# Kernel tuning notes

Hardware: AMD Instinct MI355X
Metric: run time of the kernel (lower is better)

Reference implementation:

```python
import jax, jax.numpy as jnp
import numpy as np

N_NODES = 100000


def gcn_conv(x, edge_index, W, b, num_nodes):
    """PyG GCNConv: y = D^{-1/2} (A + I) D^{-1/2} (x W) + b.

    edge_index[0] = source (row), edge_index[1] = target (col);
    messages flow source -> target with symmetric normalization.
    """
    # add self loops
    loop = jnp.arange(num_nodes, dtype=edge_index.dtype)
    row = jnp.concatenate([edge_index[0], loop])  # [E+N]
    col = jnp.concatenate([edge_index[1], loop])  # [E+N]

    xw = x @ W  # [N, F_out] -- tiny GEMM, done before gather

    # degree of target nodes (incl. self loops)
    ones = jnp.ones(col.shape[0], dtype=x.dtype)
    deg = jax.ops.segment_sum(ones, col, num_segments=num_nodes)  # [N]
    dis = jax.lax.rsqrt(jnp.maximum(deg, 1e-12))
    dis = jnp.where(deg > 0, dis, 0.0)

    norm = dis[row] * dis[col]  # [E+N]
    msg = xw[row] * norm[:, None]  # gather + scale, [E+N, F_out]
    out = jax.ops.segment_sum(msg, col, num_segments=num_nodes)  # scatter-add
    return out + b


def setup_inputs() -> dict:
    key = jax.random.key(0)
    k1, k2, k3, k4 = jax.random.split(key, 4)
    num_attr, hidden, num_classes = 128, 16, 8
    n_edges = 3200000
    x = jax.random.normal(k1, (N_NODES, num_attr), dtype=jnp.float32)
    edge_index = jax.random.randint(k2, (2, n_edges), 0, N_NODES, dtype=jnp.int64)
    W1 = jax.random.normal(k3, (num_attr, hidden), dtype=jnp.float32) / np.sqrt(num_attr)
    b1 = jnp.zeros((hidden,), dtype=jnp.float32)
    W2 = jax.random.normal(k4, (hidden, num_classes), dtype=jnp.float32) / np.sqrt(hidden)
    b2 = jnp.zeros((num_classes,), dtype=jnp.float32)
    return {"x": x, "edge_index": edge_index, "W1": W1, "b1": b1, "W2": W2, "b2": b2}


def reference(x, edge_index, W1, b1, W2, b2):
    h = gcn_conv(x, edge_index, W1, b1, N_NODES)
    h = jax.nn.relu(h)
    # dropout is identity in eval mode
    h = gcn_conv(h, edge_index, W2, b2, N_NODES)
    return jax.nn.sigmoid(h)  # [N, num_classes]
```

## Files before the change

kernel.cpp:

```cpp
#include <hip/hip_runtime.h>
#include <math.h>

static constexpr int FI = 128;
static constexpr int FH = 16;
static constexpr int FO = 8;

static constexpr int BIN_SHIFT = 8;
static constexpr int BIN_NODES = 256;
static constexpr int MAX_BINS  = 512;
static constexpr int CAPB      = 8832;
static constexpr int SCHUNK    = 8192;
static constexpr int SThreads  = 512;

__device__ __forceinline__ unsigned short f2bf(float x) {
    unsigned u = __float_as_uint(x);
    u += 0x7FFFu + ((u >> 16) & 1u);
    return (unsigned short)(u >> 16);
}
__device__ __forceinline__ float bflo(unsigned u) { return __uint_as_float(u << 16); }
__device__ __forceinline__ float bfhi(unsigned u) { return __uint_as_float(u & 0xFFFF0000u); }

__launch_bounds__(SThreads)
__global__ void k_binscatter(const int* __restrict__ row, const int* __restrict__ col,
                             int* __restrict__ binCursor, unsigned int* __restrict__ binned,
                             int E, int nbins) {
    __shared__ int lcnt[MAX_BINS];
    __shared__ int lstart[MAX_BINS];
    __shared__ int lcur[MAX_BINS];
    __shared__ int gbase[MAX_BINS];
    __shared__ int wsum[8];
    __shared__ unsigned int   staged[SCHUNK];
    __shared__ unsigned short sbin[SCHUNK];
    int t = threadIdx.x;
    int base = blockIdx.x * SCHUNK;
    int end  = base + SCHUNK; if (end > E) end = E;
    int m = end - base;
    lcnt[t] = 0;
    __syncthreads();

    int nv = m >> 2;
    const int4* c4 = (const int4*)(col + base);
    int4 creg[4];
    #pragma unroll
    for (int j = 0; j < 4; ++j) {
        int k = t + j * SThreads;
        if (k < nv) {
            creg[j] = c4[k];
            atomicAdd(&lcnt[creg[j].x >> BIN_SHIFT], 1);
            atomicAdd(&lcnt[creg[j].y >> BIN_SHIFT], 1);
            atomicAdd(&lcnt[creg[j].z >> BIN_SHIFT], 1);
            atomicAdd(&lcnt[creg[j].w >> BIN_SHIFT], 1);
        }
    }
    for (int i = base + (nv << 2) + t; i < end; i += SThreads)
        atomicAdd(&lcnt[col[i] >> BIN_SHIFT], 1);
    __syncthreads();

    int v = lcnt[t];
    int inc = v;
    #pragma unroll
    for (int d = 1; d < 64; d <<= 1) {
        int u = __shfl_up(inc, d, 64);
        if ((t & 63) >= d) inc += u;
    }
    if ((t & 63) == 63) wsum[t >> 6] = inc;
    __syncthreads();
    if (t < 8) {
        int w = wsum[t];
        #pragma unroll
        for (int d = 1; d < 8; d <<= 1) {
            int u = __shfl_up(w, d, 8);
            if (t >= d) w += u;
        }
        wsum[t] = w;
    }
    __syncthreads();
    {
        int waveoff = (t >= 64) ? wsum[(t >> 6) - 1] : 0;
        int ex = waveoff + inc - v;
        lstart[t] = ex;
        lcur[t]   = ex;
        gbase[t]  = v ? atomicAdd(&binCursor[t], v) : 0;
    }
    __syncthreads();

    const int4* r4 = (const int4*)(row + base);
    #pragma unroll
    for (int j = 0; j < 4; ++j) {
        int k = t + j * SThreads;
        if (k < nv) {
            int4 r = r4[k];
            int cc[4] = {creg[j].x, creg[j].y, creg[j].z, creg[j].w};
            int rr[4] = {r.x, r.y, r.z, r.w};
            #pragma unroll
            for (int jj = 0; jj < 4; ++jj) {
                int b = cc[jj] >> BIN_SHIFT;
                int pos = atomicAdd(&lcur[b], 1);
                staged[pos] = (unsigned)rr[jj] | ((unsigned)(cc[jj] & (BIN_NODES - 1)) << 17);
                sbin[pos] = (unsigned short)b;
            }
        }
    }
    for (int i = base + (nv << 2) + t; i < end; i += SThreads) {
        int c = col[i];
        int b = c >> BIN_SHIFT;
        int pos = atomicAdd(&lcur[b], 1);
        staged[pos] = (unsigned)row[i] | ((unsigned)(c & (BIN_NODES - 1)) << 17);
        sbin[pos] = (unsigned short)b;
    }
    __syncthreads();

    for (int i = t; i < m; i += SThreads) {
        int b = sbin[i];
        int off = gbase[b] + (i - lstart[b]);
        if (off < CAPB) binned[b * CAPB + off] = staged[i];
    }
}

__launch_bounds__(BIN_NODES)
__global__ void k_refine(const int* __restrict__ binCursor, const unsigned int* __restrict__ binned,
                         int* __restrict__ srow, int* __restrict__ starts, int* __restrict__ ends,
                         float* __restrict__ dis, int N) {
    __shared__ unsigned int  stage[CAPB];
    __shared__ unsigned char arr[CAPB];
    __shared__ int cnt[BIN_NODES];
    __shared__ int wsum[4];
    int t = threadIdx.x;
    int b = blockIdx.x;
    int s = b * CAPB;
    int m = binCursor[b];
    if (m > CAPB) m = CAPB;
    cnt[t] = 0;
    __syncthreads();

    int mm = m & ~3;
    for (int i0 = t * 4; i0 < mm; i0 += BIN_NODES * 4) {
        uint4 v = *(const uint4*)(binned + s + i0);
        *(uint4*)&stage[i0] = v;
        arr[i0 + 0] = (unsigned char)atomicAdd(&cnt[v.x >> 17], 1);
        arr[i0 + 1] = (unsigned char)atomicAdd(&cnt[v.y >> 17], 1);
        arr[i0 + 2] = (unsigned char)atomicAdd(&cnt[v.z >> 17], 1);
        arr[i0 + 3] = (unsigned char)atomicAdd(&cnt[v.w >> 17], 1);
    }
    for (int i = mm + t; i < m; i += BIN_NODES) {
        unsigned v = binned[s + i];
        stage[i] = v;
        arr[i] = (unsigned char)atomicAdd(&cnt[v >> 17], 1);
    }
    __syncthreads();

    int deg = cnt[t];
    int inc = deg;
    #pragma unroll
    for (int d = 1; d < 64; d <<= 1) {
        int u = __shfl_up(inc, d, 64);
        if ((t & 63) >= d) inc += u;
    }
    if ((t & 63) == 63) wsum[t >> 6] = inc;
    __syncthreads();
    if (t < 4) {
        int w = wsum[t];
        #pragma unroll
        for (int d = 1; d < 4; d <<= 1) {
            int u = __shfl_up(w, d, 4);
            if (t >= d) w += u;
        }
        wsum[t] = w;
    }
    __syncthreads();
    int waveoff = (t >= 64) ? wsum[(t >> 6) - 1] : 0;
    int excl = waveoff + inc - deg;

    int n = b * BIN_NODES + t;
    if (n < N) {
        starts[n] = s + excl;
        ends[n]   = s + excl + deg;
        dis[n]    = rsqrtf((float)(deg + 1));
    }
    cnt[t] = excl;
    __syncthreads();

    for (int i0 = t * 4; i0 < mm; i0 += BIN_NODES * 4) {
        uint4 v = *(uint4*)&stage[i0];
        srow[s + cnt[v.x >> 17] + arr[i0 + 0]] = v.x & 0x1FFFF;
        srow[s + cnt[v.y >> 17] + arr[i0 + 1]] = v.y & 0x1FFFF;
        srow[s + cnt[v.z >> 17] + arr[i0 + 2]] = v.z & 0x1FFFF;
        srow[s + cnt[v.w >> 17] + arr[i0 + 3]] = v.w & 0x1FFFF;
    }
    for (int i = mm + t; i < m; i += BIN_NODES) {
        unsigned v = stage[i];
        srow[s + cnt[v >> 17] + arr[i]] = v & 0x1FFFF;
    }
}

__launch_bounds__(256)
__global__ void k_gemm1(const float* __restrict__ x, const float* __restrict__ W,
                        const float* __restrict__ dis, unsigned short* __restrict__ xw1s,
                        int N) {
    __shared__ float sw[FI * FH];
    int t = threadIdx.x;
    for (int i = t; i < FI * FH; i += 256) sw[i] = W[i];
    __syncthreads();

    int nl = t >> 2;
    int f  = (t & 3) * 4;
    int n  = blockIdx.x * 64 + nl;
    if (n >= N) return;

    const float4* xr = (const float4*)(x + (size_t)n * FI);
    float a0 = 0.f, a1 = 0.f, a2 = 0.f, a3 = 0.f;
    #pragma unroll 8
    for (int kq = 0; kq < FI / 4; ++kq) {
        float4 xv = xr[kq];
        float4 w0 = *(const float4*)&sw[(kq * 4 + 0) * FH + f];
        float4 w1 = *(const float4*)&sw[(kq * 4 + 1) * FH + f];
        float4 w2 = *(const float4*)&sw[(kq * 4 + 2) * FH + f];
        float4 w3 = *(const float4*)&sw[(kq * 4 + 3) * FH + f];
        a0 = fmaf(xv.x, w0.x, a0); a1 = fmaf(xv.x, w0.y, a1);
        a2 = fmaf(xv.x, w0.z, a2); a3 = fmaf(xv.x, w0.w, a3);
        a0 = fmaf(xv.y, w1.x, a0); a1 = fmaf(xv.y, w1.y, a1);
        a2 = fmaf(xv.y, w1.z, a2); a3 = fmaf(xv.y, w1.w, a3);
        a0 = fmaf(xv.z, w2.x, a0); a1 = fmaf(xv.z, w2.y, a1);
        a2 = fmaf(xv.z, w2.z, a2); a3 = fmaf(xv.z, w2.w, a3);
        a0 = fmaf(xv.w, w3.x, a0); a1 = fmaf(xv.w, w3.y, a1);
        a2 = fmaf(xv.w, w3.z, a2); a3 = fmaf(xv.w, w3.w, a3);
    }
    float dn = dis[n];
    unsigned w0 = (unsigned)f2bf(a0 * dn) | ((unsigned)f2bf(a1 * dn) << 16);
    unsigned w1 = (unsigned)f2bf(a2 * dn) | ((unsigned)f2bf(a3 * dn) << 16);
    *(uint2*)(xw1s + (size_t)n * FH + f) = make_uint2(w0, w1);
}

__launch_bounds__(256)
__global__ void k_agg1(const int* __restrict__ starts, const int* __restrict__ ends,
                       const int* __restrict__ srow, const float* __restrict__ dis,
                       const unsigned short* __restrict__ xw1s, const float* __restrict__ W2,
                       const float* __restrict__ b1, unsigned short* __restrict__ xw2s, int N) {
    __shared__ float sw[FH * FO];
    __shared__ float sb[FH];
    int t = threadIdx.x;
    if (t < FH * FO) sw[t] = W2[t];
    if (t < FH) sb[t] = b1[t];
    __syncthreads();

    int n = blockIdx.x * 128 + (t >> 1);
    int h = t & 1;
    if (n >= N) return;
    float dn = dis[n];
    int s = starts[n], e = ends[n];
    const uint4* xq = (const uint4*)xw1s;

    uint4 sp = xq[(size_t)n * 2 + h];
    float acc[8];
    acc[0]=bflo(sp.x); acc[1]=bfhi(sp.x); acc[2]=bflo(sp.y); acc[3]=bfhi(sp.y);
    acc[4]=bflo(sp.z); acc[5]=bfhi(sp.z); acc[6]=bflo(sp.w); acc[7]=bfhi(sp.w);

    int i = s;
    for (; i + 8 <= e; i += 8) {
        int rr[8];
        #pragma unroll
        for (int j = 0; j < 8; ++j) rr[j] = srow[i + j];
        uint4 pk[8];
        #pragma unroll
        for (int j = 0; j < 8; ++j) pk[j] = xq[(size_t)rr[j] * 2 + h];
        #pragma unroll
        for (int j = 0; j < 8; ++j) {
            acc[0]+=bflo(pk[j].x); acc[1]+=bfhi(pk[j].x);
            acc[2]+=bflo(pk[j].y); acc[3]+=bfhi(pk[j].y);
            acc[4]+=bflo(pk[j].z); acc[5]+=bfhi(pk[j].z);
            acc[6]+=bflo(pk[j].w); acc[7]+=bfhi(pk[j].w);
        }
    }
    for (; i < e; ++i) {
        uint4 p = xq[(size_t)srow[i] * 2 + h];
        acc[0]+=bflo(p.x); acc[1]+=bfhi(p.x);
        acc[2]+=bflo(p.y); acc[3]+=bfhi(p.y);
        acc[4]+=bflo(p.z); acc[5]+=bfhi(p.z);
        acc[6]+=bflo(p.w); acc[7]+=bfhi(p.w);
    }

    float hv[8];
    #pragma unroll
    for (int k = 0; k < 8; ++k) {
        float v = fmaf(dn, acc[k], sb[h * 8 + k]);
        hv[k] = v > 0.f ? v : 0.f;
    }
    float po[FO];
    #pragma unroll
    for (int o = 0; o < FO; ++o) {
        float a = 0.f;
        #pragma unroll
        for (int k = 0; k < 8; ++k) a = fmaf(hv[k], sw[(h * 8 + k) * FO + o], a);
        po[o] = a;
    }
    #pragma unroll
    for (int o = 0; o < FO; ++o) po[o] += __shfl_xor(po[o], 1, 64);
    int o0 = h * 4;
    unsigned w0 = (unsigned)f2bf(po[o0 + 0] * dn) | ((unsigned)f2bf(po[o0 + 1] * dn) << 16);
    unsigned w1 = (unsigned)f2bf(po[o0 + 2] * dn) | ((unsigned)f2bf(po[o0 + 3] * dn) << 16);
    *(uint2*)(xw2s + (size_t)n * FO + o0) = make_uint2(w0, w1);
}

__launch_bounds__(256)
__global__ void k_agg2(const int* __restrict__ starts, const int* __restrict__ ends,
                       const int* __restrict__ srow, const float* __restrict__ dis,
                       const unsigned short* __restrict__ xw2s, const float* __restrict__ b2,
                       float* __restrict__ out, int N) {
    int t = threadIdx.x;
    int n = blockIdx.x * 128 + (t >> 1);
    int h = t & 1;
    if (n >= N) return;
    float dn = dis[n];
    int s = starts[n], e = ends[n];
    const uint2* xq = (const uint2*)xw2s;

    uint2 sp = xq[(size_t)n * 2 + h];
    float acc[4];
    acc[0]=bflo(sp.x); acc[1]=bfhi(sp.x); acc[2]=bflo(sp.y); acc[3]=bfhi(sp.y);

    int i = s;
    for (; i + 8 <= e; i += 8) {
        int rr[8];
        #pragma unroll
        for (int j = 0; j < 8; ++j) rr[j] = srow[i + j];
        uint2 pk[8];
        #pragma unroll
        for (int j = 0; j < 8; ++j) pk[j] = xq[(size_t)rr[j] * 2 + h];
        #pragma unroll
        for (int j = 0; j < 8; ++j) {
            acc[0]+=bflo(pk[j].x); acc[1]+=bfhi(pk[j].x);
            acc[2]+=bflo(pk[j].y); acc[3]+=bfhi(pk[j].y);
        }
    }
    for (; i < e; ++i) {
        uint2 p = xq[(size_t)srow[i] * 2 + h];
        acc[0]+=bflo(p.x); acc[1]+=bfhi(p.x);
        acc[2]+=bflo(p.y); acc[3]+=bfhi(p.y);
    }

    int f0 = h * 4;
    float r[4];
    #pragma unroll
    for (int k = 0; k < 4; ++k) {
        float v = fmaf(dn, acc[k], b2[f0 + k]);
        r[k] = 1.f / (1.f + __expf(-v));
    }
    *(float4*)(out + (size_t)n * FO + f0) = make_float4(r[0], r[1], r[2], r[3]);
}

extern "C" void kernel_launch(void* const* d_in, const int* in_sizes, int n_in,
                              void* d_out, int out_size, void* d_ws, size_t ws_size,
                              hipStream_t stream) {
    const float* x  = (const float*)d_in[0];
    const int*   ei = (const int*)d_in[1];
    const float* W1 = (const float*)d_in[2];
    const float* b1 = (const float*)d_in[3];
    const float* W2 = (const float*)d_in[4];
    const float* b2 = (const float*)d_in[5];

    const int N = in_sizes[0] / FI;
    const int E = in_sizes[1] / 2;
    const int* row = ei;
    const int* col = ei + E;
    const int nbins = (N + BIN_NODES - 1) >> BIN_SHIFT;

    const size_t NP = 100352;
    const size_t BINSZ = (size_t)nbins * CAPB;
    float* base = (float*)d_ws;
    int*   starts    = (int*)base;
    int*   ends      = (int*)(base + NP);
    float* dis       = base + 2 * NP;
    int*   binCursor = (int*)(base + 3 * NP);
    unsigned int* binned = (unsigned int*)(base + 3 * NP + 1024);
    int*   srow      = (int*)(base + 3 * NP + 1024 + BINSZ);
    unsigned short* xw1s = (unsigned short*)(base + 3 * NP + 1024 + 2 * BINSZ);
    unsigned short* xw2s = (unsigned short*)(base + 3 * NP + 1024 + 2 * BINSZ + NP * 8);
    float* out = (float*)d_out;

    size_t needed = (3 * NP + 1024 + 2 * BINSZ + NP * 12) * 4;
    if (ws_size < needed) return;

    hipMemsetAsync(binCursor, 0, (size_t)nbins * sizeof(int), stream);
    k_binscatter<<<(E + SCHUNK - 1) / SCHUNK, SThreads,  0, stream>>>(row, col, binCursor, binned, E, nbins);
    k_refine    <<<nbins, BIN_NODES,                     0, stream>>>(binCursor, binned, srow, starts, ends, dis, N);
    k_gemm1     <<<(N + 63) / 64, 256,                   0, stream>>>(x, W1, dis, xw1s, N);
    k_agg1      <<<(2 * N + 255) / 256, 256,             0, stream>>>(starts, ends, srow, dis, xw1s, W2, b1, xw2s, N);
    k_agg2      <<<(2 * N + 255) / 256, 256,             0, stream>>>(starts, ends, srow, dis, xw2s, b2, out, N);
}
```

Before: 122.2 us.

## Fuse layer-1 GEMM into edge binning kernel and apply degree scaling in refine

The separate GEMM launch is gone. Its work now runs as extra blocks of the bin-scatter kernel, sharing a shared-memory union, so the dense x@W1 pass overlaps with edge binning. Because degrees are not known yet at that point, the GEMM writes unscaled bf16 values. The refine kernel then rescales each node's row by its D^-1/2 factor. This removes one launch and hides the GEMM's memory traffic, but adds an extra read-modify-write of xw1 and a second bf16 rounding.

```diff
diff --git a/kernel.cpp b/kernel.cpp
--- a/kernel.cpp
+++ b/kernel.cpp
@@ -20,22 +20,61 @@
 __device__ __forceinline__ float bflo(unsigned u) { return __uint_as_float(u << 16); }
 __device__ __forceinline__ float bfhi(unsigned u) { return __uint_as_float(u & 0xFFFF0000u); }
 
+struct SMemScatter {
+    int lcnt[MAX_BINS];
+    int lstart[MAX_BINS];
+    int lcur[MAX_BINS];
+    int gbase[MAX_BINS];
+    int wsum[8];
+    unsigned int   staged[SCHUNK];
+    unsigned short sbin[SCHUNK];
+};
+struct SMemGemm { float sw[FI * FH]; };
+union SMemU { SMemScatter s; SMemGemm g; };
+
 __launch_bounds__(SThreads)
-__global__ void k_binscatter(const int* __restrict__ row, const int* __restrict__ col,
-                             int* __restrict__ binCursor, unsigned int* __restrict__ binned,
-                             int E, int nbins) {
-    __shared__ int lcnt[MAX_BINS];
-    __shared__ int lstart[MAX_BINS];
-    __shared__ int lcur[MAX_BINS];
-    __shared__ int gbase[MAX_BINS];
-    __shared__ int wsum[8];
-    __shared__ unsigned int   staged[SCHUNK];
-    __shared__ unsigned short sbin[SCHUNK];
+__global__ void k_scatter_gemm(const int* __restrict__ row, const int* __restrict__ col,
+                               int* __restrict__ binCursor, unsigned int* __restrict__ binned,
+                               const float* __restrict__ x, const float* __restrict__ W1,
+                               unsigned short* __restrict__ xw1, int E, int nchunks, int N) {
+    __shared__ SMemU sm;
     int t = threadIdx.x;
+
+    if ((int)blockIdx.x >= nchunks) {
+        for (int i = t; i < FI * FH; i += SThreads) sm.g.sw[i] = W1[i];
+        __syncthreads();
+        int nl = t >> 2;
+        int f  = (t & 3) * 4;
+        int n  = ((int)blockIdx.x - nchunks) * 128 + nl;
+        if (n >= N) return;
+        const float4* xr = (const float4*)(x + (size_t)n * FI);
+        float a0 = 0.f, a1 = 0.f, a2 = 0.f, a3 = 0.f;
+        #pragma unroll 8
+        for (int kq = 0; kq < FI / 4; ++kq) {
+            float4 xv = xr[kq];
+            float4 w0 = *(const float4*)&sm.g.sw[(kq * 4 + 0) * FH + f];
+            float4 w1 = *(const float4*)&sm.g.sw[(kq * 4 + 1) * FH + f];
+            float4 w2 = *(const float4*)&sm.g.sw[(kq * 4 + 2) * FH + f];
+            float4 w3 = *(const float4*)&sm.g.sw[(kq * 4 + 3) * FH + f];
+            a0 = fmaf(xv.x, w0.x, a0); a1 = fmaf(xv.x, w0.y, a1);
+            a2 = fmaf(xv.x, w0.z, a2); a3 = fmaf(xv.x, w0.w, a3);
+            a0 = fmaf(xv.y, w1.x, a0); a1 = fmaf(xv.y, w1.y, a1);
+            a2 = fmaf(xv.y, w1.z, a2); a3 = fmaf(xv.y, w1.w, a3);
+            a0 = fmaf(xv.z, w2.x, a0); a1 = fmaf(xv.z, w2.y, a1);
+            a2 = fmaf(xv.z, w2.z, a2); a3 = fmaf(xv.z, w2.w, a3);
+            a0 = fmaf(xv.w, w3.x, a0); a1 = fmaf(xv.w, w3.y, a1);
+            a2 = fmaf(xv.w, w3.z, a2); a3 = fmaf(xv.w, w3.w, a3);
+        }
+        unsigned w0 = (unsigned)f2bf(a0) | ((unsigned)f2bf(a1) << 16);
+        unsigned w1 = (unsigned)f2bf(a2) | ((unsigned)f2bf(a3) << 16);
+        *(uint2*)(xw1 + (size_t)n * FH + f) = make_uint2(w0, w1);
+        return;
+    }
+
     int base = blockIdx.x * SCHUNK;
     int end  = base + SCHUNK; if (end > E) end = E;
     int m = end - base;
-    lcnt[t] = 0;
+    sm.s.lcnt[t] = 0;
     __syncthreads();
 
     int nv = m >> 2;
@@ -46,41 +85,41 @@
         int k = t + j * SThreads;
         if (k < nv) {
             creg[j] = c4[k];
-            atomicAdd(&lcnt[creg[j].x >> BIN_SHIFT], 1);
-            atomicAdd(&lcnt[creg[j].y >> BIN_SHIFT], 1);
-            atomicAdd(&lcnt[creg[j].z >> BIN_SHIFT], 1);
-            atomicAdd(&lcnt[creg[j].w >> BIN_SHIFT], 1);
+            atomicAdd(&sm.s.lcnt[creg[j].x >> BIN_SHIFT], 1);
+            atomicAdd(&sm.s.lcnt[creg[j].y >> BIN_SHIFT], 1);
+            atomicAdd(&sm.s.lcnt[creg[j].z >> BIN_SHIFT], 1);
+            atomicAdd(&sm.s.lcnt[creg[j].w >> BIN_SHIFT], 1);
         }
     }
     for (int i = base + (nv << 2) + t; i < end; i += SThreads)
-        atomicAdd(&lcnt[col[i] >> BIN_SHIFT], 1);
-    __syncthreads();
-
-    int v = lcnt[t];
+        atomicAdd(&sm.s.lcnt[col[i] >> BIN_SHIFT], 1);
+    __syncthreads();
+
+    int v = sm.s.lcnt[t];
     int inc = v;
     #pragma unroll
     for (int d = 1; d < 64; d <<= 1) {
         int u = __shfl_up(inc, d, 64);
         if ((t & 63) >= d) inc += u;
     }
-    if ((t & 63) == 63) wsum[t >> 6] = inc;
+    if ((t & 63) == 63) sm.s.wsum[t >> 6] = inc;
     __syncthreads();
     if (t < 8) {
-        int w = wsum[t];
+        int w = sm.s.wsum[t];
         #pragma unroll
         for (int d = 1; d < 8; d <<= 1) {
             int u = __shfl_up(w, d, 8);
             if (t >= d) w += u;
         }
-        wsum[t] = w;
+        sm.s.wsum[t] = w;
     }
     __syncthreads();
     {
-        int waveoff = (t >= 64) ? wsum[(t >> 6) - 1] : 0;
+        int waveoff = (t >= 64) ? sm.s.wsum[(t >> 6) - 1] : 0;
         int ex = waveoff + inc - v;
-        lstart[t] = ex;
-        lcur[t]   = ex;
-        gbase[t]  = v ? atomicAdd(&binCursor[t], v) : 0;
+        sm.s.lstart[t] = ex;
+        sm.s.lcur[t]   = ex;
+        sm.s.gbase[t]  = v ? atomicAdd(&binCursor[t], v) : 0;
     }
     __syncthreads();
 
@@ -95,32 +134,32 @@
             #pragma unroll
             for (int jj = 0; jj < 4; ++jj) {
                 int b = cc[jj] >> BIN_SHIFT;
-                int pos = atomicAdd(&lcur[b], 1);
-                staged[pos] = (unsigned)rr[jj] | ((unsigned)(cc[jj] & (BIN_NODES - 1)) << 17);
-                sbin[pos] = (unsigned short)b;
+                int pos = atomicAdd(&sm.s.lcur[b], 1);
+                sm.s.staged[pos] = (unsigned)rr[jj] | ((unsigned)(cc[jj] & (BIN_NODES - 1)) << 17);
+                sm.s.sbin[pos] = (unsigned short)b;
             }
         }
     }
     for (int i = base + (nv << 2) + t; i < end; i += SThreads) {
         int c = col[i];
         int b = c >> BIN_SHIFT;
-        int pos = atomicAdd(&lcur[b], 1);
-        staged[pos] = (unsigned)row[i] | ((unsigned)(c & (BIN_NODES - 1)) << 17);
-        sbin[pos] = (unsigned short)b;
+        int pos = atomicAdd(&sm.s.lcur[b], 1);
+        sm.s.staged[pos] = (unsigned)row[i] | ((unsigned)(c & (BIN_NODES - 1)) << 17);
+        sm.s.sbin[pos] = (unsigned short)b;
     }
     __syncthreads();
 
     for (int i = t; i < m; i += SThreads) {
-        int b = sbin[i];
-        int off = gbase[b] + (i - lstart[b]);
-        if (off < CAPB) binned[b * CAPB + off] = staged[i];
+        int b = sm.s.sbin[i];
+        int off = sm.s.gbase[b] + (i - sm.s.lstart[b]);
+        if (off < CAPB) binned[b * CAPB + off] = sm.s.staged[i];
     }
 }
 
 __launch_bounds__(BIN_NODES)
 __global__ void k_refine(const int* __restrict__ binCursor, const unsigned int* __restrict__ binned,
                          int* __restrict__ srow, int* __restrict__ starts, int* __restrict__ ends,
-                         float* __restrict__ dis, int N) {
+                         float* __restrict__ dis, unsigned short* __restrict__ xw1, int N) {
     __shared__ unsigned int  stage[CAPB];
     __shared__ unsigned char arr[CAPB];
     __shared__ int cnt[BIN_NODES];
@@ -172,10 +211,11 @@
     int excl = waveoff + inc - deg;
 
     int n = b * BIN_NODES + t;
+    float dv = rsqrtf((float)(deg + 1));
     if (n < N) {
         starts[n] = s + excl;
         ends[n]   = s + excl + deg;
-        dis[n]    = rsqrtf((float)(deg + 1));
+        dis[n]    = dv;
     }
     cnt[t] = excl;
     __syncthreads();
@@ -191,44 +231,20 @@
         unsigned v = stage[i];
         srow[s + cnt[v >> 17] + arr[i]] = v & 0x1FFFF;
     }
-}
-
-__launch_bounds__(256)
-__global__ void k_gemm1(const float* __restrict__ x, const float* __restrict__ W,
-                        const float* __restrict__ dis, unsigned short* __restrict__ xw1s,
-                        int N) {
-    __shared__ float sw[FI * FH];
-    int t = threadIdx.x;
-    for (int i = t; i < FI * FH; i += 256) sw[i] = W[i];
-    __syncthreads();
-
-    int nl = t >> 2;
-    int f  = (t & 3) * 4;
-    int n  = blockIdx.x * 64 + nl;
-    if (n >= N) return;
-
-    const float4* xr = (const float4*)(x + (size_t)n * FI);
-    float a0 = 0.f, a1 = 0.f, a2 = 0.f, a3 = 0.f;
-    #pragma unroll 8
-    for (int kq = 0; kq < FI / 4; ++kq) {
-        float4 xv = xr[kq];
-        float4 w0 = *(const float4*)&sw[(kq * 4 + 0) * FH + f];
-        float4 w1 = *(const float4*)&sw[(kq * 4 + 1) * FH + f];
-        float4 w2 = *(const float4*)&sw[(kq * 4 + 2) * FH + f];
-        float4 w3 = *(const float4*)&sw[(kq * 4 + 3) * FH + f];
-        a0 = fmaf(xv.x, w0.x, a0); a1 = fmaf(xv.x, w0.y, a1);
-        a2 = fmaf(xv.x, w0.z, a2); a3 = fmaf(xv.x, w0.w, a3);
-        a0 = fmaf(xv.y, w1.x, a0); a1 = fmaf(xv.y, w1.y, a1);
-        a2 = fmaf(xv.y, w1.z, a2); a3 = fmaf(xv.y, w1.w, a3);
-        a0 = fmaf(xv.z, w2.x, a0); a1 = fmaf(xv.z, w2.y, a1);
-        a2 = fmaf(xv.z, w2.z, a2); a3 = fmaf(xv.z, w2.w, a3);
-        a0 = fmaf(xv.w, w3.x, a0); a1 = fmaf(xv.w, w3.y, a1);
-        a2 = fmaf(xv.w, w3.z, a2); a3 = fmaf(xv.w, w3.w, a3);
-    }
-    float dn = dis[n];
-    unsigned w0 = (unsigned)f2bf(a0 * dn) | ((unsigned)f2bf(a1 * dn) << 16);
-    unsigned w1 = (unsigned)f2bf(a2 * dn) | ((unsigned)f2bf(a3 * dn) << 16);
-    *(uint2*)(xw1s + (size_t)n * FH + f) = make_uint2(w0, w1);
+
+    if (n < N) {
+        uint4* p = (uint4*)(xw1 + (size_t)n * FH);
+        uint4 va = p[0], vb = p[1];
+        unsigned* u = &va.x;
+        #pragma unroll
+        for (int k = 0; k < 4; ++k)
+            u[k] = (unsigned)f2bf(bflo(u[k]) * dv) | ((unsigned)f2bf(bfhi(u[k]) * dv) << 16);
+        unsigned* w = &vb.x;
+        #pragma unroll
+        for (int k = 0; k < 4; ++k)
+            w[k] = (unsigned)f2bf(bflo(w[k]) * dv) | ((unsigned)f2bf(bfhi(w[k]) * dv) << 16);
+        p[0] = va; p[1] = vb;
+    }
 }
 
 __launch_bounds__(256)
@@ -364,6 +380,9 @@
     const int* col = ei + E;
     const int nbins = (N + BIN_NODES - 1) >> BIN_SHIFT;
 
+    const int nchunks = (E + SCHUNK - 1) / SCHUNK;
+    const int ngemm   = (N + 127) / 128;
+
     const size_t NP = 100352;
     const size_t BINSZ = (size_t)nbins * CAPB;
     float* base = (float*)d_ws;
@@ -381,9 +400,9 @@
     if (ws_size < needed) return;
 
     hipMemsetAsync(binCursor, 0, (size_t)nbins * sizeof(int), stream);
-    k_binscatter<<<(E + SCHUNK - 1) / SCHUNK, SThreads,  0, stream>>>(row, col, binCursor, binned, E, nbins);
-    k_refine    <<<nbins, BIN_NODES,                     0, stream>>>(binCursor, binned, srow, starts, ends, dis, N);
-    k_gemm1     <<<(N + 63) / 64, 256,                   0, stream>>>(x, W1, dis, xw1s, N);
-    k_agg1      <<<(2 * N + 255) / 256, 256,             0, stream>>>(starts, ends, srow, dis, xw1s, W2, b1, xw2s, N);
-    k_agg2      <<<(2 * N + 255) / 256, 256,             0, stream>>>(starts, ends, srow, dis, xw2s, b2, out, N);
-}
+    k_scatter_gemm<<<nchunks + ngemm, SThreads, 0, stream>>>(row, col, binCursor, binned,
+                                                             x, W1, xw1s, E, nchunks, N);
+    k_refine      <<<nbins, BIN_NODES,          0, stream>>>(binCursor, binned, srow, starts, ends, dis, xw1s, N);
+    k_agg1        <<<(2 * N + 255) / 256, 256,  0, stream>>>(starts, ends, srow, dis, xw1s, W2, b1, xw2s, N);
+    k_agg2        <<<(2 * N + 255) / 256, 256,  0, stream>>>(starts, ends, srow, dis, xw2s, b2, out, N);
+}
```

New measurement: 119.7 us. 1.02x faster.
